# Kernel optimization log

Hardware: AMD Instinct MI355X
Metric: run time of the kernel (lower is better)

## Reference

```python
import jax, jax.numpy as jnp
import numpy as np
import math

B, T, C = 4, 4096, 1024
N_HEAD = 16
N_GROUPS = 16  # must equal n_head for the original torch matmul to broadcast
WINDOW = 256
ROPE_BASE = 10000.0


def _rope(x):
    # x: [B, H, T, D] -- rotate interleaved pairs along last dim, positions along T
    D = x.shape[-1]
    Tn = x.shape[2]
    inv_freq = 1.0 / (ROPE_BASE ** (jnp.arange(0, D, 2, dtype=jnp.float32) / D))  # [D/2]
    ang = jnp.arange(Tn, dtype=jnp.float32)[:, None] * inv_freq[None, :]          # [T, D/2]
    cos, sin = jnp.cos(ang), jnp.sin(ang)
    x1, x2 = x[..., 0::2], x[..., 1::2]
    y1 = x1 * cos - x2 * sin
    y2 = x1 * sin + x2 * cos
    return jnp.stack([y1, y2], axis=-1).reshape(x.shape)


def setup_inputs() -> dict:
    key = jax.random.key(0)
    k1, k2, k3 = jax.random.split(key, 3)
    x = jax.random.normal(k1, (B, T, C), dtype=jnp.float32)
    W_in = jax.random.normal(k2, (C, 3 * C), dtype=jnp.float32) * 0.02
    b_in = jnp.zeros((3 * C,), dtype=jnp.float32)
    W_out = jax.random.normal(k3, (C, C), dtype=jnp.float32) * 0.02
    b_out = jnp.zeros((C,), dtype=jnp.float32)
    return {"x": x, "W_in": W_in, "b_in": b_in, "W_out": W_out, "b_out": b_out}


def reference(x, W_in, b_in, W_out, b_out):
    b, t, c = x.shape
    H, G, W = N_HEAD, N_GROUPS, WINDOW
    hd = c // H          # query head dim
    kd = c // G          # kv head dim (== hd since G == H)
    qkv = x @ W_in + b_in
    q, k, v = jnp.split(qkv, 3, axis=-1)
    q = q.reshape(b, t, H, hd).transpose(0, 2, 1, 3)   # [B,H,T,hd]
    k = k.reshape(b, t, G, kd).transpose(0, 2, 1, 3)   # [B,G,T,kd]
    v = v.reshape(b, t, G, kd).transpose(0, 2, 1, 3)
    q = _rope(q)
    k = _rope(k)
    nW = t // W
    qw = q.reshape(b, H, nW, W, hd)
    kw = k.reshape(b, G, nW, W, kd)
    vw = v.reshape(b, G, nW, W, kd)
    scale = 1.0 / math.sqrt(kd)
    att = jnp.einsum('bhnqd,bhnkd->bhnqk', qw, kw) * scale  # block-local scores
    att = jax.nn.softmax(att, axis=-1)
    yw = jnp.einsum('bhnqk,bhnkd->bhnqd', att, vw)
    y = yw.reshape(b, H, t, hd).transpose(0, 2, 1, 3).reshape(b, t, c)
    return y @ W_out + b_out
```

## Files before the change

### kernel.cpp

```cpp
#include <hip/hip_runtime.h>
#include <math.h>

#define T_SEQ 4096
#define CDIM  1024
#define WIN   256

#define ROPE_C 0.415241012f
#define SCALE_LOG2E 0.1803368801f

typedef __attribute__((ext_vector_type(8))) short short8;
typedef __attribute__((ext_vector_type(4))) float float4v;

__device__ __forceinline__ unsigned int f2bf(float f) {
  unsigned int u = __float_as_uint(f);
  u += 0x7fffu + ((u >> 16) & 1u);
  return u >> 16;
}

__device__ __forceinline__ void gload16(const unsigned short* g, unsigned short* l) {
  __builtin_amdgcn_global_load_lds(
      (__attribute__((address_space(1))) void*)g,
      (__attribute__((address_space(3))) void*)l, 16, 0, 0);
}

__global__ __launch_bounds__(256)
void rope_tab(float2* __restrict__ tab) {
  const int i = blockIdx.x * 256 + threadIdx.x;
  const int tpos = i >> 5, pi = i & 31;
  const float ang = (float)tpos * exp2f(-(float)pi * ROPE_C);
  tab[i] = make_float2(cosf(ang), sinf(ang));
}

__global__ __launch_bounds__(256)
void perm_bias(const float* __restrict__ b, float* __restrict__ pb) {
  const int n = blockIdx.x * 256 + threadIdx.x;
  int np = n;
  if (n < 2 * CDIM) np = (n & ~63) | ((n & 1) * 32) | ((n & 63) >> 1);
  pb[np] = b[n];
}

__global__ __launch_bounds__(256)
void cvt_f32_bf16(const float* __restrict__ src, unsigned short* __restrict__ dst) {
  const long i = ((long)blockIdx.x * 256 + threadIdx.x) * 8;
  float4 u0 = *(const float4*)(src + i);
  float4 u1 = *(const float4*)(src + i + 4);
  uint4 pk;
  pk.x = f2bf(u0.x) | (f2bf(u0.y) << 16);
  pk.y = f2bf(u0.z) | (f2bf(u0.w) << 16);
  pk.z = f2bf(u1.x) | (f2bf(u1.y) << 16);
  pk.w = f2bf(u1.z) | (f2bf(u1.w) << 16);
  *(uint4*)(dst + i) = pk;
}

__global__ __launch_bounds__(256)
void transpose_cvt(const float* __restrict__ W, unsigned short* __restrict__ dst,
                   int K, int N, int permqk) {
  __shared__ float tile[32][33];
  const int tid = threadIdx.x;
  const int ktile = blockIdx.y * 32, ntile = blockIdx.x * 32;
  const int kl = tid >> 3, nl4 = (tid & 7) * 4;
  float4 v = *(const float4*)&W[(size_t)(ktile + kl) * N + ntile + nl4];
  tile[nl4 + 0][kl] = v.x;
  tile[nl4 + 1][kl] = v.y;
  tile[nl4 + 2][kl] = v.z;
  tile[nl4 + 3][kl] = v.w;
  __syncthreads();
  const int nl = tid >> 3, kl4 = (tid & 7) * 4;
  uint2 pk;
  pk.x = f2bf(tile[nl][kl4 + 0]) | (f2bf(tile[nl][kl4 + 1]) << 16);
  pk.y = f2bf(tile[nl][kl4 + 2]) | (f2bf(tile[nl][kl4 + 3]) << 16);
  int n = ntile + nl;
  if (permqk && n < 2 * CDIM) n = (n & ~63) | ((n & 1) * 32) | ((n & 63) >> 1);
  long i = (long)n * K + ktile + kl4;
  *(uint2*)(dst + i) = pk;
}

__global__ __launch_bounds__(256, 5)
void gemm_bf16(const unsigned short* __restrict__ A,
               const unsigned short* __restrict__ Bt,
               const float* __restrict__ bias,
               const float2* __restrict__ ropetab,
               void* __restrict__ Cp, int ldc, int K, int mode, int nbx) {
  __shared__ unsigned short As[128 * 32];
  __shared__ unsigned short Bs[128 * 32];
  const int t = threadIdx.x;
  const int nwg = gridDim.x;
  const int cpx = nwg >> 3;
  const int wg = blockIdx.x;
  const int swz = (wg & 7) * cpx + (wg >> 3);
  const int row0 = (swz / nbx) * 128, col0 = (swz % nbx) * 128;
  const int lane = t & 63, wave = t >> 6;
  const int wm = (wave >> 1) * 64, wn = (wave & 1) * 64;
  const int l15 = lane & 15, quad = lane >> 4;

  const int sr = t >> 2;
  const int sc = (t & 3) ^ ((sr >> 1) & 3);
  const unsigned short* a0 = A + (size_t)(row0 + sr) * K + sc * 8;
  const unsigned short* b0 = Bt + (size_t)(col0 + sr) * K + sc * 8;
  unsigned short* la = &As[t * 8];
  unsigned short* lb = &Bs[t * 8];

  float4v acc[4][4];
#pragma unroll
  for (int i = 0; i < 4; ++i)
#pragma unroll
    for (int j = 0; j < 4; ++j) acc[i][j] = (float4v){0.f, 0.f, 0.f, 0.f};

  for (int k0 = 0; k0 < K; k0 += 32) {
    __syncthreads();
    gload16(a0 + k0, la);
    gload16(a0 + (size_t)64 * K + k0, la + 2048);
    gload16(b0 + k0, lb);
    gload16(b0 + (size_t)64 * K + k0, lb + 2048);
    asm volatile("s_waitcnt vmcnt(0)" ::: "memory");
    __syncthreads();

    short8 af[4], bfr[4];
#pragma unroll
    for (int mt = 0; mt < 4; ++mt) {
      const int r = wm + mt * 16 + l15;
      af[mt] = *(const short8*)&As[r * 32 + ((quad ^ ((r >> 1) & 3)) * 8)];
    }
#pragma unroll
    for (int nt = 0; nt < 4; ++nt) {
      const int r = wn + nt * 16 + l15;
      bfr[nt] = *(const short8*)&Bs[r * 32 + ((quad ^ ((r >> 1) & 3)) * 8)];
    }
#pragma unroll
    for (int mt = 0; mt < 4; ++mt)
#pragma unroll
      for (int nt = 0; nt < 4; ++nt)
        acc[mt][nt] = __builtin_amdgcn_mfma_f32_16x16x32_bf16(af[mt], bfr[nt],
                                                              acc[mt][nt], 0, 0, 0);
  }

  if (mode) {
    unsigned short* co = (unsigned short*)Cp;
    if (col0 < 2 * CDIM) {
      float bb1[2], bb2[2];
#pragma unroll
      for (int ntp = 0; ntp < 2; ++ntp) {
        bb1[ntp] = bias[col0 + wn + ntp * 16 + l15];
        bb2[ntp] = bias[col0 + wn + ntp * 16 + l15 + 32];
      }
#pragma unroll
      for (int mt = 0; mt < 4; ++mt) {
#pragma unroll
        for (int r = 0; r < 4; ++r) {
          const int row = row0 + wm + mt * 16 + quad * 4 + r;
          const float2* tb = &ropetab[(size_t)(row & (T_SEQ - 1)) * 32];
          unsigned short* rp0 = co + (size_t)row * ldc + col0 + wn;
#pragma unroll
          for (int ntp = 0; ntp < 2; ++ntp) {
            const float2 cs = tb[ntp * 16 + l15];
            const float x1 = acc[mt][ntp][r] + bb1[ntp];
            const float x2 = acc[mt][ntp + 2][r] + bb2[ntp];
            const float y1 = x1 * cs.x - x2 * cs.y;
            const float y2 = x1 * cs.y + x2 * cs.x;
            const float y1p = __shfl_xor(y1, 1);
            const float y2p = __shfl_xor(y2, 1);
            if (!(l15 & 1)) {
              *(unsigned int*)(rp0 + ntp * 16 + l15) = f2bf(y1) | (f2bf(y1p) << 16);
              *(unsigned int*)(rp0 + ntp * 16 + l15 + 32) = f2bf(y2) | (f2bf(y2p) << 16);
            }
          }
        }
      }
    } else {
      float bb[4];
#pragma unroll
      for (int nt = 0; nt < 4; ++nt) bb[nt] = bias[col0 + wn + nt * 16 + l15];
#pragma unroll
      for (int mt = 0; mt < 4; ++mt) {
#pragma unroll
        for (int r = 0; r < 4; ++r) {
          const int row = row0 + wm + mt * 16 + quad * 4 + r;
          unsigned short* rp0 = co + (size_t)row * ldc + col0 + wn;
#pragma unroll
          for (int nt = 0; nt < 4; ++nt) {
            const float v = acc[mt][nt][r] + bb[nt];
            const float vp = __shfl_xor(v, 1);
            if (!(l15 & 1))
              *(unsigned int*)(rp0 + nt * 16 + l15) = f2bf(v) | (f2bf(vp) << 16);
          }
        }
      }
    }
  } else {
    float* co = (float*)Cp;
    float bb[4];
#pragma unroll
    for (int nt = 0; nt < 4; ++nt) bb[nt] = bias[col0 + wn + nt * 16 + l15];
#pragma unroll
    for (int mt = 0; mt < 4; ++mt) {
#pragma unroll
      for (int r = 0; r < 4; ++r) {
        const int row = row0 + wm + mt * 16 + quad * 4 + r;
        float* rp0 = co + (size_t)row * ldc + col0 + wn;
#pragma unroll
        for (int nt = 0; nt < 4; ++nt)
          rp0[nt * 16 + l15] = acc[mt][nt][r] + bb[nt];
      }
    }
  }
}

__global__ __launch_bounds__(256, 2)
void attn_mfma(const unsigned short* __restrict__ qkv, unsigned short* __restrict__ Y) {
  __shared__ unsigned short Ks[128 * 64];
  __shared__ unsigned short Vt[64 * 128];
  __shared__ unsigned short Ps[4][64 * 32];

  const int w = blockIdx.x, h = blockIdx.y, b = blockIdx.z;
  const int t = threadIdx.x;
  const int lane = t & 63, wv = t >> 6;
  const int l15 = lane & 15, quad = lane >> 4;
  const int t0 = w * WIN;
  const size_t base = ((size_t)b * T_SEQ + t0) * 3072;

  short8 qf[4][2];
#pragma unroll
  for (int mt = 0; mt < 4; ++mt) {
    const unsigned short* qp = qkv + base + (size_t)(wv * 64 + mt * 16 + l15) * 3072 + h * 64;
#pragma unroll
    for (int ks = 0; ks < 2; ++ks)
      qf[mt][ks] = *(const short8*)(qp + ks * 32 + quad * 8);
  }

  float4v accy[4][4];
#pragma unroll
  for (int i = 0; i < 4; ++i)
#pragma unroll
    for (int j = 0; j < 4; ++j) accy[i][j] = (float4v){0.f, 0.f, 0.f, 0.f};
  float m_[4][4], l_[4][4];
#pragma unroll
  for (int i = 0; i < 4; ++i)
#pragma unroll
    for (int j = 0; j < 4; ++j) { m_[i][j] = -3.0e38f; l_[i][j] = 0.f; }

  for (int half = 0; half < 2; ++half) {
    if (half) __syncthreads();
    {
      const int kr = t >> 3, kc = t & 7;
      const unsigned short* kp = qkv + base + (size_t)(half * 128 + kr) * 3072 + 1024 +
                                 h * 64 + ((kc ^ (kr & 7)) * 8);
      unsigned short* lp = &Ks[t * 8];
#pragma unroll
      for (int p = 0; p < 4; ++p)
        gload16(kp + (size_t)p * 32 * 3072, lp + p * 2048);
    }
    {
      const int kpair = 2 * (t & 63);
      const int d0 = (t >> 6) * 16;
      const unsigned short* v0 = qkv + base + (size_t)(half * 128 + kpair) * 3072 + 2048 +
                                 h * 64 + d0;
      const unsigned short* v1 = v0 + 3072;
      short8 a0[2], a1[2];
#pragma unroll
      for (int j = 0; j < 2; ++j) {
        a0[j] = *(const short8*)(v0 + j * 8);
        a1[j] = *(const short8*)(v1 + j * 8);
      }
      const int c = kpair >> 3;
#pragma unroll
      for (int j = 0; j < 2; ++j)
#pragma unroll
        for (int e = 0; e < 8; ++e) {
          const int d = d0 + 8 * j + e;
          const unsigned int pk = (unsigned int)(unsigned short)a0[j][e] |
                                  ((unsigned int)(unsigned short)a1[j][e] << 16);
          *(unsigned int*)&Vt[d * 128 + ((c ^ (d & 7)) * 8) + (kpair & 7)] = pk;
        }
    }
    asm volatile("s_waitcnt vmcnt(0)" ::: "memory");
    __syncthreads();

    for (int kc = 0; kc < 4; ++kc) {
      short8 kf[2][2];
#pragma unroll
      for (int nt = 0; nt < 2; ++nt)
#pragma unroll
        for (int ks = 0; ks < 2; ++ks) {
          const int r = kc * 32 + nt * 16 + l15;
          const int c = ks * 4 + quad;
          kf[nt][ks] = *(const short8*)&Ks[r * 64 + ((c ^ (l15 & 7)) * 8)];
        }
      float4v s_[4][2];
#pragma unroll
      for (int mt = 0; mt < 4; ++mt)
#pragma unroll
        for (int nt = 0; nt < 2; ++nt) {
          s_[mt][nt] = __builtin_amdgcn_mfma_f32_16x16x32_bf16(
              qf[mt][0], kf[nt][0], (float4v){0.f, 0.f, 0.f, 0.f}, 0, 0, 0);
          s_[mt][nt] = __builtin_amdgcn_mfma_f32_16x16x32_bf16(
              qf[mt][1], kf[nt][1], s_[mt][nt], 0, 0, 0);
        }
#pragma unroll
      for (int mt = 0; mt < 4; ++mt) {
#pragma unroll
        for (int reg = 0; reg < 4; ++reg) {
          float s0 = s_[mt][0][reg] * SCALE_LOG2E;
          float s1 = s_[mt][1][reg] * SCALE_LOG2E;
          float mx = fmaxf(s0, s1);
          mx = fmaxf(mx, __shfl_xor(mx, 1));
          mx = fmaxf(mx, __shfl_xor(mx, 2));
          mx = fmaxf(mx, __shfl_xor(mx, 4));
          mx = fmaxf(mx, __shfl_xor(mx, 8));
          const float mn = fmaxf(m_[mt][reg], mx);
          const float al = exp2f(m_[mt][reg] - mn);
          const float p0 = exp2f(s0 - mn);
          const float p1 = exp2f(s1 - mn);
          float ps = p0 + p1;
          ps += __shfl_xor(ps, 1);
          ps += __shfl_xor(ps, 2);
          ps += __shfl_xor(ps, 4);
          ps += __shfl_xor(ps, 8);
          l_[mt][reg] = l_[mt][reg] * al + ps;
          m_[mt][reg] = mn;
#pragma unroll
          for (int dt = 0; dt < 4; ++dt) accy[mt][dt][reg] *= al;
          const float q0 = __shfl_xor(p0, 1);
          const float q1 = __shfl_xor(p1, 1);
          const unsigned int w0 = f2bf(p0) | (f2bf(q0) << 16);
          const unsigned int w1 = f2bf(p1) | (f2bf(q1) << 16);
          if (!(l15 & 1)) {
            const int row = mt * 16 + quad * 4 + reg;
            const int ca = (0 + (l15 >> 3)) ^ (row & 3);
            const int cb = (2 + (l15 >> 3)) ^ (row & 3);
            *(unsigned int*)&Ps[wv][row * 32 + ca * 8 + (l15 & 7)] = w0;
            *(unsigned int*)&Ps[wv][row * 32 + cb * 8 + (l15 & 7)] = w1;
          }
        }
      }
      short8 pf[4], vf[4];
#pragma unroll
      for (int mt = 0; mt < 4; ++mt) {
        const int row = mt * 16 + l15;
        pf[mt] = *(const short8*)&Ps[wv][row * 32 + ((quad ^ (l15 & 3)) * 8)];
      }
#pragma unroll
      for (int dt = 0; dt < 4; ++dt) {
        const int d = dt * 16 + l15;
        const int c = kc * 4 + quad;
        vf[dt] = *(const short8*)&Vt[d * 128 + ((c ^ (d & 7)) * 8)];
      }
#pragma unroll
      for (int mt = 0; mt < 4; ++mt)
#pragma unroll
        for (int dt = 0; dt < 4; ++dt)
          accy[mt][dt] = __builtin_amdgcn_mfma_f32_16x16x32_bf16(pf[mt], vf[dt],
                                                                 accy[mt][dt], 0, 0, 0);
    }
  }

#pragma unroll
  for (int mt = 0; mt < 4; ++mt) {
#pragma unroll
    for (int reg = 0; reg < 4; ++reg) {
      const float rl = 1.f / l_[mt][reg];
      const int row = wv * 64 + mt * 16 + quad * 4 + reg;
      unsigned short* yp = Y + ((size_t)b * T_SEQ + t0 + row) * CDIM + h * 64;
#pragma unroll
      for (int dt = 0; dt < 4; ++dt) {
        const float y = accy[mt][dt][reg] * rl;
        const float ypart = __shfl_xor(y, 1);
        if (!(l15 & 1))
          *(unsigned int*)(yp + dt * 16 + l15) = f2bf(y) | (f2bf(ypart) << 16);
      }
    }
  }
}

extern "C" void kernel_launch(void* const* d_in, const int* in_sizes, int n_in,
                              void* d_out, int out_size, void* d_ws, size_t ws_size,
                              hipStream_t stream) {
  const float* x     = (const float*)d_in[0];
  const float* W_in  = (const float*)d_in[1];
  const float* b_in  = (const float*)d_in[2];
  const float* W_out = (const float*)d_in[3];
  const float* b_out = (const float*)d_in[4];
  float* out = (float*)d_out;
  char* ws = (char*)d_ws;
  unsigned short* qkvb  = (unsigned short*)ws;
  unsigned short* Abf   = (unsigned short*)(ws + (96u << 20));
  unsigned short* Ybf   = (unsigned short*)(ws + (128u << 20));
  unsigned short* WinT  = (unsigned short*)(ws + (160u << 20));
  unsigned short* WoutT = (unsigned short*)(ws + (166u << 20));
  float2* ropetabp      = (float2*)(ws + (168u << 20));
  float* pbias          = (float*)(ws + (169u << 20));

  rope_tab<<<512, 256, 0, stream>>>(ropetabp);
  perm_bias<<<12, 256, 0, stream>>>(b_in, pbias);
  cvt_f32_bf16<<<8192, 256, 0, stream>>>(x, Abf);
  transpose_cvt<<<dim3(3072 / 32, 1024 / 32), 256, 0, stream>>>(W_in, WinT, 1024, 3072, 1);
  transpose_cvt<<<dim3(1024 / 32, 1024 / 32), 256, 0, stream>>>(W_out, WoutT, 1024, 1024, 0);
  gemm_bf16<<<dim3(24 * 128), 256, 0, stream>>>(
      Abf, WinT, pbias, ropetabp, qkvb, 3 * CDIM, CDIM, 1, 24);
  attn_mfma<<<dim3(T_SEQ / WIN, 16, 4), 256, 0, stream>>>(qkvb, Ybf);
  gemm_bf16<<<dim3(8 * 128), 256, 0, stream>>>(
      Ybf, WoutT, b_out, nullptr, out, CDIM, CDIM, 0, 8);
}
```

Before: 443.3 us.

## Double-buffer GEMM LDS tiles and add lazy rescaling to online softmax

The bf16 GEMM main loop now uses two LDS buffers. The global-to-LDS load for the next K slice is issued before the MFMA compute on the current slice, which removes the explicit vmcnt wait and one barrier per step so load latency can overlap compute. The attention softmax skips the max update and the rescaling of accumulator and denominator when every lane's new max stays within 8 (log2 units) of the running max, avoiding exp2 calls and multiplies in the common case. The trade-offs are doubled LDS use, which may cut occupancy under launch_bounds 5, and a wave-wide vote branch in the softmax. Correctness of the GEMM relies on the implicit wait that __syncthreads provides before a buffer is reused.

```diff
diff --git a/kernel.cpp b/kernel.cpp
--- a/kernel.cpp
+++ b/kernel.cpp
@@ -81,8 +81,10 @@
                const float* __restrict__ bias,
                const float2* __restrict__ ropetab,
                void* __restrict__ Cp, int ldc, int K, int mode, int nbx) {
-  __shared__ unsigned short As[128 * 32];
-  __shared__ unsigned short Bs[128 * 32];
+  __shared__ unsigned short As0[128 * 32];
+  __shared__ unsigned short Bs0[128 * 32];
+  __shared__ unsigned short As1[128 * 32];
+  __shared__ unsigned short Bs1[128 * 32];
   const int t = threadIdx.x;
   const int nwg = gridDim.x;
   const int cpx = nwg >> 3;
@@ -97,8 +99,6 @@
   const int sc = (t & 3) ^ ((sr >> 1) & 3);
   const unsigned short* a0 = A + (size_t)(row0 + sr) * K + sc * 8;
   const unsigned short* b0 = Bt + (size_t)(col0 + sr) * K + sc * 8;
-  unsigned short* la = &As[t * 8];
-  unsigned short* lb = &Bs[t * 8];
 
   float4v acc[4][4];
 #pragma unroll
@@ -106,25 +106,23 @@
 #pragma unroll
     for (int j = 0; j < 4; ++j) acc[i][j] = (float4v){0.f, 0.f, 0.f, 0.f};
 
-  for (int k0 = 0; k0 < K; k0 += 32) {
-    __syncthreads();
-    gload16(a0 + k0, la);
-    gload16(a0 + (size_t)64 * K + k0, la + 2048);
-    gload16(b0 + k0, lb);
-    gload16(b0 + (size_t)64 * K + k0, lb + 2048);
-    asm volatile("s_waitcnt vmcnt(0)" ::: "memory");
-    __syncthreads();
-
+  auto stage = [&](unsigned short* As_, unsigned short* Bs_, int k0) {
+    gload16(a0 + k0, &As_[t * 8]);
+    gload16(a0 + (size_t)64 * K + k0, &As_[t * 8 + 2048]);
+    gload16(b0 + k0, &Bs_[t * 8]);
+    gload16(b0 + (size_t)64 * K + k0, &Bs_[t * 8 + 2048]);
+  };
+  auto compute = [&](const unsigned short* As_, const unsigned short* Bs_) {
     short8 af[4], bfr[4];
 #pragma unroll
     for (int mt = 0; mt < 4; ++mt) {
       const int r = wm + mt * 16 + l15;
-      af[mt] = *(const short8*)&As[r * 32 + ((quad ^ ((r >> 1) & 3)) * 8)];
+      af[mt] = *(const short8*)&As_[r * 32 + ((quad ^ ((r >> 1) & 3)) * 8)];
     }
 #pragma unroll
     for (int nt = 0; nt < 4; ++nt) {
       const int r = wn + nt * 16 + l15;
-      bfr[nt] = *(const short8*)&Bs[r * 32 + ((quad ^ ((r >> 1) & 3)) * 8)];
+      bfr[nt] = *(const short8*)&Bs_[r * 32 + ((quad ^ ((r >> 1) & 3)) * 8)];
     }
 #pragma unroll
     for (int mt = 0; mt < 4; ++mt)
@@ -132,7 +130,22 @@
       for (int nt = 0; nt < 4; ++nt)
         acc[mt][nt] = __builtin_amdgcn_mfma_f32_16x16x32_bf16(af[mt], bfr[nt],
                                                               acc[mt][nt], 0, 0, 0);
+  };
+
+  stage(As0, Bs0, 0);
+  __syncthreads();
+  for (int k0 = 0; k0 < K - 64; k0 += 64) {
+    stage(As1, Bs1, k0 + 32);
+    compute(As0, Bs0);
+    __syncthreads();
+    stage(As0, Bs0, k0 + 64);
+    compute(As1, Bs1);
+    __syncthreads();
   }
+  stage(As1, Bs1, K - 32);
+  compute(As0, Bs0);
+  __syncthreads();
+  compute(As1, Bs1);
 
   if (mode) {
     unsigned short* co = (unsigned short*)Cp;
@@ -306,19 +319,27 @@
           mx = fmaxf(mx, __shfl_xor(mx, 2));
           mx = fmaxf(mx, __shfl_xor(mx, 4));
           mx = fmaxf(mx, __shfl_xor(mx, 8));
-          const float mn = fmaxf(m_[mt][reg], mx);
-          const float al = exp2f(m_[mt][reg] - mn);
-          const float p0 = exp2f(s0 - mn);
-          const float p1 = exp2f(s1 - mn);
+          const float m_old = m_[mt][reg];
+          float p0, p1;
+          if (__all(mx <= m_old + 8.f)) {
+            p0 = exp2f(s0 - m_old);
+            p1 = exp2f(s1 - m_old);
+          } else {
+            const float mn = fmaxf(m_old, mx);
+            const float al = exp2f(m_old - mn);
+            p0 = exp2f(s0 - mn);
+            p1 = exp2f(s1 - mn);
+            l_[mt][reg] *= al;
+            m_[mt][reg] = mn;
+#pragma unroll
+            for (int dt = 0; dt < 4; ++dt) accy[mt][dt][reg] *= al;
+          }
           float ps = p0 + p1;
           ps += __shfl_xor(ps, 1);
           ps += __shfl_xor(ps, 2);
           ps += __shfl_xor(ps, 4);
           ps += __shfl_xor(ps, 8);
-          l_[mt][reg] = l_[mt][reg] * al + ps;
-          m_[mt][reg] = mn;
-#pragma unroll
-          for (int dt = 0; dt < 4; ++dt) accy[mt][dt][reg] *= al;
+          l_[mt][reg] += ps;
           const float q0 = __shfl_xor(p0, 1);
           const float q1 = __shfl_xor(p1, 1);
           const unsigned int w0 = f2bf(p0) | (f2bf(q0) << 16);
```

Measured after the change: 656.9 us. 1.48x slower.

## Transpose attention score MFMA so softmax reductions stay in-lane, add lazy rescale

Applied to the files above, without the earlier changes.

Computes scores as K·Q^T so each lane holds one query's values across keys. Row max and sum then need only two cross-quad shuffles instead of many 16-lane shuffle chains per register. Adds a wave-uniform conditional that skips the rescale of the accumulator and running sum when the new max stays within a threshold of the old one. Repacks P and the output through LDS so global stores are 16-byte vectors. This adds per-tile LDS round-trips, and stale-max exponentials can grow by up to 2^8 before renormalisation.

```diff
diff --git a/kernel.cpp b/kernel.cpp
--- a/kernel.cpp
+++ b/kernel.cpp
@@ -209,7 +209,7 @@
 void attn_mfma(const unsigned short* __restrict__ qkv, unsigned short* __restrict__ Y) {
   __shared__ unsigned short Ks[128 * 64];
   __shared__ unsigned short Vt[64 * 128];
-  __shared__ unsigned short Ps[4][64 * 32];
+  __shared__ unsigned short Ps[4][2048];
 
   const int w = blockIdx.x, h = blockIdx.y, b = blockIdx.z;
   const int t = threadIdx.x;
@@ -220,11 +220,11 @@
 
   short8 qf[4][2];
 #pragma unroll
-  for (int mt = 0; mt < 4; ++mt) {
-    const unsigned short* qp = qkv + base + (size_t)(wv * 64 + mt * 16 + l15) * 3072 + h * 64;
+  for (int qt = 0; qt < 4; ++qt) {
+    const unsigned short* qp = qkv + base + (size_t)(wv * 64 + qt * 16 + l15) * 3072 + h * 64;
 #pragma unroll
     for (int ks = 0; ks < 2; ++ks)
-      qf[mt][ks] = *(const short8*)(qp + ks * 32 + quad * 8);
+      qf[qt][ks] = *(const short8*)(qp + ks * 32 + quad * 8);
   }
 
   float4v accy[4][4];
@@ -232,11 +232,9 @@
   for (int i = 0; i < 4; ++i)
 #pragma unroll
     for (int j = 0; j < 4; ++j) accy[i][j] = (float4v){0.f, 0.f, 0.f, 0.f};
-  float m_[4][4], l_[4][4];
-#pragma unroll
-  for (int i = 0; i < 4; ++i)
-#pragma unroll
-    for (int j = 0; j < 4; ++j) { m_[i][j] = -3.0e38f; l_[i][j] = 0.f; }
+  float m_[4], l_[4];
+#pragma unroll
+  for (int i = 0; i < 4; ++i) { m_[i] = -3.0e38f; l_[i] = 0.f; }
 
   for (int half = 0; half < 2; ++half) {
     if (half) __syncthreads();
@@ -278,96 +276,97 @@
     for (int kc = 0; kc < 4; ++kc) {
       short8 kf[2][2];
 #pragma unroll
-      for (int nt = 0; nt < 2; ++nt)
+      for (int kt = 0; kt < 2; ++kt)
 #pragma unroll
         for (int ks = 0; ks < 2; ++ks) {
-          const int r = kc * 32 + nt * 16 + l15;
+          const int r = kc * 32 + kt * 16 + l15;
           const int c = ks * 4 + quad;
-          kf[nt][ks] = *(const short8*)&Ks[r * 64 + ((c ^ (l15 & 7)) * 8)];
+          kf[kt][ks] = *(const short8*)&Ks[r * 64 + ((c ^ (l15 & 7)) * 8)];
         }
-      float4v s_[4][2];
-#pragma unroll
-      for (int mt = 0; mt < 4; ++mt)
-#pragma unroll
-        for (int nt = 0; nt < 2; ++nt) {
-          s_[mt][nt] = __builtin_amdgcn_mfma_f32_16x16x32_bf16(
-              qf[mt][0], kf[nt][0], (float4v){0.f, 0.f, 0.f, 0.f}, 0, 0, 0);
-          s_[mt][nt] = __builtin_amdgcn_mfma_f32_16x16x32_bf16(
-              qf[mt][1], kf[nt][1], s_[mt][nt], 0, 0, 0);
-        }
-#pragma unroll
-      for (int mt = 0; mt < 4; ++mt) {
-#pragma unroll
-        for (int reg = 0; reg < 4; ++reg) {
-          float s0 = s_[mt][0][reg] * SCALE_LOG2E;
-          float s1 = s_[mt][1][reg] * SCALE_LOG2E;
-          float mx = fmaxf(s0, s1);
-          mx = fmaxf(mx, __shfl_xor(mx, 1));
-          mx = fmaxf(mx, __shfl_xor(mx, 2));
-          mx = fmaxf(mx, __shfl_xor(mx, 4));
-          mx = fmaxf(mx, __shfl_xor(mx, 8));
-          const float mn = fmaxf(m_[mt][reg], mx);
-          const float al = exp2f(m_[mt][reg] - mn);
-          const float p0 = exp2f(s0 - mn);
-          const float p1 = exp2f(s1 - mn);
-          float ps = p0 + p1;
-          ps += __shfl_xor(ps, 1);
-          ps += __shfl_xor(ps, 2);
-          ps += __shfl_xor(ps, 4);
-          ps += __shfl_xor(ps, 8);
-          l_[mt][reg] = l_[mt][reg] * al + ps;
-          m_[mt][reg] = mn;
-#pragma unroll
-          for (int dt = 0; dt < 4; ++dt) accy[mt][dt][reg] *= al;
-          const float q0 = __shfl_xor(p0, 1);
-          const float q1 = __shfl_xor(p1, 1);
-          const unsigned int w0 = f2bf(p0) | (f2bf(q0) << 16);
-          const unsigned int w1 = f2bf(p1) | (f2bf(q1) << 16);
-          if (!(l15 & 1)) {
-            const int row = mt * 16 + quad * 4 + reg;
-            const int ca = (0 + (l15 >> 3)) ^ (row & 3);
-            const int cb = (2 + (l15 >> 3)) ^ (row & 3);
-            *(unsigned int*)&Ps[wv][row * 32 + ca * 8 + (l15 & 7)] = w0;
-            *(unsigned int*)&Ps[wv][row * 32 + cb * 8 + (l15 & 7)] = w1;
-          }
-        }
-      }
-      short8 pf[4], vf[4];
-#pragma unroll
-      for (int mt = 0; mt < 4; ++mt) {
-        const int row = mt * 16 + l15;
-        pf[mt] = *(const short8*)&Ps[wv][row * 32 + ((quad ^ (l15 & 3)) * 8)];
-      }
+      short8 vf[4];
 #pragma unroll
       for (int dt = 0; dt < 4; ++dt) {
         const int d = dt * 16 + l15;
         const int c = kc * 4 + quad;
         vf[dt] = *(const short8*)&Vt[d * 128 + ((c ^ (d & 7)) * 8)];
       }
-#pragma unroll
-      for (int mt = 0; mt < 4; ++mt)
+
+#pragma unroll
+      for (int qt = 0; qt < 4; ++qt) {
+        float4v sT0 = __builtin_amdgcn_mfma_f32_16x16x32_bf16(
+            kf[0][0], qf[qt][0], (float4v){0.f, 0.f, 0.f, 0.f}, 0, 0, 0);
+        sT0 = __builtin_amdgcn_mfma_f32_16x16x32_bf16(kf[0][1], qf[qt][1], sT0, 0, 0, 0);
+        float4v sT1 = __builtin_amdgcn_mfma_f32_16x16x32_bf16(
+            kf[1][0], qf[qt][0], (float4v){0.f, 0.f, 0.f, 0.f}, 0, 0, 0);
+        sT1 = __builtin_amdgcn_mfma_f32_16x16x32_bf16(kf[1][1], qf[qt][1], sT1, 0, 0, 0);
+
+        float s0 = sT0[0] * SCALE_LOG2E, s1 = sT0[1] * SCALE_LOG2E;
+        float s2 = sT0[2] * SCALE_LOG2E, s3 = sT0[3] * SCALE_LOG2E;
+        float s4 = sT1[0] * SCALE_LOG2E, s5 = sT1[1] * SCALE_LOG2E;
+        float s6 = sT1[2] * SCALE_LOG2E, s7 = sT1[3] * SCALE_LOG2E;
+
+        float mx = fmaxf(fmaxf(fmaxf(s0, s1), fmaxf(s2, s3)),
+                         fmaxf(fmaxf(s4, s5), fmaxf(s6, s7)));
+        mx = fmaxf(mx, __shfl_xor(mx, 16));
+        mx = fmaxf(mx, __shfl_xor(mx, 32));
+
+        const float m_old = m_[qt];
+        float p0, p1, p2, p3, p4, p5, p6, p7;
+        if (__all(mx <= m_old + 8.f)) {
+          p0 = exp2f(s0 - m_old); p1 = exp2f(s1 - m_old);
+          p2 = exp2f(s2 - m_old); p3 = exp2f(s3 - m_old);
+          p4 = exp2f(s4 - m_old); p5 = exp2f(s5 - m_old);
+          p6 = exp2f(s6 - m_old); p7 = exp2f(s7 - m_old);
+        } else {
+          const float mn = fmaxf(m_old, mx);
+          const float al = exp2f(m_old - mn);
+          p0 = exp2f(s0 - mn); p1 = exp2f(s1 - mn);
+          p2 = exp2f(s2 - mn); p3 = exp2f(s3 - mn);
+          p4 = exp2f(s4 - mn); p5 = exp2f(s5 - mn);
+          p6 = exp2f(s6 - mn); p7 = exp2f(s7 - mn);
+          l_[qt] *= al;
+          m_[qt] = mn;
+#pragma unroll
+          for (int dt = 0; dt < 4; ++dt) accy[dt][qt] *= al;
+        }
+        float ps = ((p0 + p1) + (p2 + p3)) + ((p4 + p5) + (p6 + p7));
+        ps += __shfl_xor(ps, 16);
+        ps += __shfl_xor(ps, 32);
+        l_[qt] += ps;
+
+        unsigned short* pw = &Ps[wv][l15 * 40];
+        *(unsigned int*)&pw[0 * 16 + quad * 4 + 0] = f2bf(p0) | (f2bf(p1) << 16);
+        *(unsigned int*)&pw[0 * 16 + quad * 4 + 2] = f2bf(p2) | (f2bf(p3) << 16);
+        *(unsigned int*)&pw[1 * 16 + quad * 4 + 0] = f2bf(p4) | (f2bf(p5) << 16);
+        *(unsigned int*)&pw[1 * 16 + quad * 4 + 2] = f2bf(p6) | (f2bf(p7) << 16);
+        short8 pb = *(const short8*)&Ps[wv][l15 * 40 + quad * 8];
 #pragma unroll
         for (int dt = 0; dt < 4; ++dt)
-          accy[mt][dt] = __builtin_amdgcn_mfma_f32_16x16x32_bf16(pf[mt], vf[dt],
-                                                                 accy[mt][dt], 0, 0, 0);
+          accy[dt][qt] = __builtin_amdgcn_mfma_f32_16x16x32_bf16(vf[dt], pb,
+                                                                accy[dt][qt], 0, 0, 0);
+      }
     }
   }
 
 #pragma unroll
-  for (int mt = 0; mt < 4; ++mt) {
-#pragma unroll
-    for (int reg = 0; reg < 4; ++reg) {
-      const float rl = 1.f / l_[mt][reg];
-      const int row = wv * 64 + mt * 16 + quad * 4 + reg;
-      unsigned short* yp = Y + ((size_t)b * T_SEQ + t0 + row) * CDIM + h * 64;
-#pragma unroll
-      for (int dt = 0; dt < 4; ++dt) {
-        const float y = accy[mt][dt][reg] * rl;
-        const float ypart = __shfl_xor(y, 1);
-        if (!(l15 & 1))
-          *(unsigned int*)(yp + dt * 16 + l15) = f2bf(y) | (f2bf(ypart) << 16);
-      }
-    }
+  for (int qt = 0; qt < 4; ++qt) {
+    const float rl = 1.f / l_[qt];
+    unsigned short* ew = &Ps[wv][l15 * 72];
+#pragma unroll
+    for (int dt = 0; dt < 4; ++dt) {
+      const float y0 = accy[dt][qt][0] * rl;
+      const float y1 = accy[dt][qt][1] * rl;
+      const float y2 = accy[dt][qt][2] * rl;
+      const float y3 = accy[dt][qt][3] * rl;
+      *(unsigned int*)&ew[dt * 16 + quad * 4 + 0] = f2bf(y0) | (f2bf(y1) << 16);
+      *(unsigned int*)&ew[dt * 16 + quad * 4 + 2] = f2bf(y2) | (f2bf(y3) << 16);
+    }
+    const int row = wv * 64 + qt * 16 + l15;
+    unsigned short* yp = Y + ((size_t)b * T_SEQ + t0 + row) * CDIM + h * 64 + quad * 16;
+    uint4 v0 = *(const uint4*)&Ps[wv][l15 * 72 + quad * 16];
+    uint4 v1 = *(const uint4*)&Ps[wv][l15 * 72 + quad * 16 + 8];
+    *(uint4*)yp = v0;
+    *(uint4*)(yp + 8) = v1;
   }
 }
 
```

After: 375.7 us. 1.18x faster.
